# Performance work log

Measured on AMD Instinct MI355X. Metric: run time of the kernel, lower is better.

The kernel has to match this reference:

```python
import jax, jax.numpy as jnp
import numpy as np

D_MODEL = 1024
N_HEADS = 16
HEAD_DIM = D_MODEL // N_HEADS
D_FF = 4096
ROPE_RANK = 16
LN_EPS = 1e-5


def _ln(x, g, b):
    mu = jnp.mean(x, axis=-1, keepdims=True)
    var = jnp.mean((x - mu) ** 2, axis=-1, keepdims=True)
    return (x - mu) * jax.lax.rsqrt(var + LN_EPS) * g + b


def _rope(x, A, B_):
    # x: [B, T, D]; learned low-rank additive correction to sin/cos tables
    B, T, D = x.shape
    pos = jnp.arange(T, dtype=jnp.float32)
    theta = 1.0 / (10000.0 ** (jnp.arange(0, D, 2, dtype=jnp.float32) / D))  # [D/2]
    angles = pos[:, None] * theta[None, :]                                   # [T, D/2]
    sin_pos, cos_pos = jnp.sin(angles), jnp.cos(angles)
    base = jnp.concatenate([sin_pos, cos_pos], axis=-1)                      # [T, D]
    learned = (base @ A) @ B_                                                # [T, D]
    l_sin, l_cos = jnp.split(learned, 2, axis=-1)
    sin_f = sin_pos + l_sin                                                  # [T, D/2]
    cos_f = cos_pos + l_cos
    xe, xo = x[..., ::2], x[..., 1::2]
    re = xe * cos_f[None] - xo * sin_f[None]
    ro = xe * sin_f[None] + xo * cos_f[None]
    return jnp.stack([re, ro], axis=-1).reshape(B, T, D)


def setup_inputs() -> dict:
    key = jax.random.key(0)
    ks = jax.random.split(key, 20)
    B, T = 2, 2048
    s = 1.0 / np.sqrt(D_MODEL)
    sf = 1.0 / np.sqrt(D_FF)
    sr = 1.0 / np.sqrt(ROPE_RANK)
    return {
        "tgt": jax.random.normal(ks[0], (B, T, D_MODEL), jnp.float32),
        "Wq": jax.random.normal(ks[1], (D_MODEL, D_MODEL), jnp.float32) * s,
        "bq": jnp.zeros((D_MODEL,), jnp.float32),
        "Wk": jax.random.normal(ks[2], (D_MODEL, D_MODEL), jnp.float32) * s,
        "bk": jnp.zeros((D_MODEL,), jnp.float32),
        "Wv": jax.random.normal(ks[3], (D_MODEL, D_MODEL), jnp.float32) * s,
        "bv": jnp.zeros((D_MODEL,), jnp.float32),
        "Wo": jax.random.normal(ks[4], (D_MODEL, D_MODEL), jnp.float32) * s,
        "bo": jnp.zeros((D_MODEL,), jnp.float32),
        "W1": jax.random.normal(ks[5], (D_MODEL, D_FF), jnp.float32) * s,
        "b1": jnp.zeros((D_FF,), jnp.float32),
        "W2": jax.random.normal(ks[6], (D_FF, D_MODEL), jnp.float32) * sf,
        "b2": jnp.zeros((D_MODEL,), jnp.float32),
        "ln1_g": jnp.ones((D_MODEL,), jnp.float32),
        "ln1_b": jnp.zeros((D_MODEL,), jnp.float32),
        "ln2_g": jnp.ones((D_MODEL,), jnp.float32),
        "ln2_b": jnp.zeros((D_MODEL,), jnp.float32),
        "rope_A": jax.random.normal(ks[7], (D_MODEL, ROPE_RANK), jnp.float32) * s,
        "rope_B": jax.random.normal(ks[8], (ROPE_RANK, D_MODEL), jnp.float32) * sr,
    }


def reference(tgt, Wq, bq, Wk, bk, Wv, bv, Wo, bo, W1, b1, W2, b2,
              ln1_g, ln1_b, ln2_g, ln2_b, rope_A, rope_B):
    x = tgt
    B, T, D = x.shape
    q = _rope(x @ Wq + bq, rope_A, rope_B)
    k = _rope(x @ Wk + bk, rope_A, rope_B)
    v = x @ Wv + bv
    # [B, H, T, hd]
    q = q.reshape(B, T, N_HEADS, HEAD_DIM).transpose(0, 2, 1, 3)
    k = k.reshape(B, T, N_HEADS, HEAD_DIM).transpose(0, 2, 1, 3)
    v = v.reshape(B, T, N_HEADS, HEAD_DIM).transpose(0, 2, 1, 3)
    scores = jnp.einsum("bhqd,bhkd->bhqk", q, k) / np.sqrt(HEAD_DIM)
    attn = jax.nn.softmax(scores, axis=-1)  # no mask: module applies none
    ctx = jnp.einsum("bhqk,bhkd->bhqd", attn, v)
    ctx = ctx.transpose(0, 2, 1, 3).reshape(B, T, D)
    x = x + (ctx @ Wo + bo)
    x = _ln(x, ln1_g, ln1_b)
    ff = jax.nn.relu(x @ W1 + b1) @ W2 + b2
    x = _ln(x + ff, ln2_g, ln2_b)
    return x
```

## Files before the change

### kernel.cpp

```cpp
#include <hip/hip_runtime.h>
#include <math.h>

typedef unsigned short u16;
typedef unsigned int u32;
typedef __attribute__((ext_vector_type(8))) short short8v;
typedef __attribute__((ext_vector_type(4))) float f32x4;

__device__ __forceinline__ u16 f2bf(float f) {
    u32 u = __float_as_uint(f);
    u32 r = (u + 0x7fffu + ((u >> 16) & 1u)) >> 16;
    return (u16)r;
}

#define GLOAD_LDS(g, l)                                                        \
    __builtin_amdgcn_global_load_lds(                                          \
        (const __attribute__((address_space(1))) void*)(g),                    \
        (__attribute__((address_space(3))) void*)(l), 16, 0, 0)

#define SCHED_FENCE() __builtin_amdgcn_sched_barrier(0)

__global__ void cast_k(const float* __restrict__ x, u16* __restrict__ y) {
    const int gid = blockIdx.x * blockDim.x + threadIdx.x;
    float4 v = ((const float4*)x)[gid];
    ushort4 o;
    o.x = f2bf(v.x); o.y = f2bf(v.y); o.z = f2bf(v.z); o.w = f2bf(v.w);
    ((ushort4*)y)[gid] = o;
}

__global__ __launch_bounds__(256) void tcast_k(const float* __restrict__ S,
                                               u16* __restrict__ Dt,
                                               int K, int N) {
    __shared__ float tile[32][33];
    const int n0 = blockIdx.x * 32, k0 = blockIdx.y * 32;
    const int tx = threadIdx.x & 31, ty = threadIdx.x >> 5;
#pragma unroll
    for (int i = 0; i < 4; i++)
        tile[ty + 8 * i][tx] = S[(size_t)(k0 + ty + 8 * i) * N + n0 + tx];
    __syncthreads();
#pragma unroll
    for (int i = 0; i < 4; i++)
        Dt[(size_t)(n0 + ty + 8 * i) * K + k0 + tx] = f2bf(tile[tx][ty + 8 * i]);
}

__global__ __launch_bounds__(256) void vtrans_k(const u16* __restrict__ vv,
                                                u16* __restrict__ Vt) {
    __shared__ u16 tile[32][33];
    const int key0 = blockIdx.x * 32, d0 = blockIdx.y * 32, bh = blockIdx.z;
    const int b = bh >> 4, h = bh & 15;
    const int tx = threadIdx.x & 31, ty = threadIdx.x >> 5;
#pragma unroll
    for (int i = 0; i < 4; i++)
        tile[ty + 8 * i][tx] =
            vv[(size_t)(b * 2048 + key0 + ty + 8 * i) * 1024 + h * 64 + d0 + tx];
    __syncthreads();
#pragma unroll
    for (int i = 0; i < 4; i++) {
        const int d = d0 + ty + 8 * i;
        const int key = key0 + tx;
        const int ksw = (key & ~63) | ((((key >> 3) & 7) ^ (d & 7)) << 3) | (key & 7);
        Vt[((size_t)bh * 64 + d) * 2048 + ksw] = tile[tx][ty + 8 * i];
    }
}

#define ROPE_LOG2C (13.287712379549449f / 512.0f)

__global__ __launch_bounds__(256) void rope1_k(const float* __restrict__ A,
                                               float* __restrict__ P) {
    __shared__ float sc[16][17];
    __shared__ float cc[16][17];
    __shared__ float Als[16][17];
    __shared__ float Alc[16][17];
    const int tid = threadIdx.x;
    const int tt = tid >> 4, rr = tid & 15;
    const int t = blockIdx.x * 16 + tt;
    float acc = 0.f;
    for (int i0 = 0; i0 < 512; i0 += 16) {
        __syncthreads();
        {
            const int i = i0 + rr;
            const float th = exp2f(-(float)i * ROPE_LOG2C);
            const float ang = (float)t * th;
            sc[tt][rr] = sinf(ang);
            cc[tt][rr] = cosf(ang);
            Als[tt][rr] = A[(i0 + tt) * 16 + rr];
            Alc[tt][rr] = A[(512 + i0 + tt) * 16 + rr];
        }
        __syncthreads();
#pragma unroll
        for (int ii = 0; ii < 16; ++ii)
            acc = fmaf(sc[tt][ii], Als[ii][rr],
                       fmaf(cc[tt][ii], Alc[ii][rr], acc));
    }
    P[t * 16 + rr] = acc;
}

__global__ void rope2_k(const float* __restrict__ P, const float* __restrict__ Bw,
                        float* __restrict__ sf, float* __restrict__ cf) {
    const int gid = blockIdx.x * blockDim.x + threadIdx.x;
    if (gid >= 2048 * 512) return;
    const int t = gid >> 9, i = gid & 511;
    float ls = 0.f, lc = 0.f;
#pragma unroll
    for (int r = 0; r < 16; ++r) {
        const float p = P[t * 16 + r];
        ls = fmaf(p, Bw[r * 1024 + i], ls);
        lc = fmaf(p, Bw[r * 1024 + 512 + i], lc);
    }
    const float th = exp2f(-(float)i * ROPE_LOG2C);
    const float ang = (float)t * th;
    sf[gid] = sinf(ang) + ls;
    cf[gid] = cosf(ang) + lc;
}

__device__ __forceinline__ void xcd_tile(int L, int xn, int rn, int rm,
                                         int& tm, int& tn) {
    const int xcd = L & 7, i = L >> 3;
    const int cx = xcd % xn, cy = xcd / xn;
    tn = cx * rn + (i % rn);
    tm = cy * rm + (i / rn);
}

enum { EP_NONE = 0, EP_RES = 2, EP_RELU = 3 };

template <int EPI, bool CBF, int BN>
__global__ __launch_bounds__(256) void mgemm_k(
    const u16* __restrict__ A, const u16* __restrict__ Bt,
    const float* __restrict__ bias, const float* __restrict__ resf,
    void* __restrict__ Cp, int M, int N, int K, int xn, int rn, int rm) {
    constexpr int NT = BN / 32;
    __shared__ u16 As[3 * 128 * 32];
    __shared__ u16 Bs[3 * BN * 32];
    const int tid = threadIdx.x;
    const int w = tid >> 6, l = tid & 63;
    const int quad = l >> 4, lr = l & 15;
    const int wr = w >> 1, wc = w & 1;
    int tm, tn;
    xcd_tile(blockIdx.x, xn, rn, rm, tm, tn);
    const int m0 = tm * 128, n0 = tn * BN;

    const int srow = w * 16 + (l >> 2);
    const int scol = (((l & 3) ^ ((l >> 3) & 3)) * 8);
    const u16* ag0 = A + (size_t)(m0 + srow) * K + scol;
    const u16* ag1 = A + (size_t)(m0 + 64 + srow) * K + scol;
    const u16* bg0 = Bt + (size_t)(n0 + srow) * K + scol;
    const u16* bg1 = Bt + (size_t)(n0 + 64 + srow) * K + scol;

    f32x4 acc[4][NT];
#pragma unroll
    for (int i = 0; i < 4; i++)
#pragma unroll
        for (int j = 0; j < NT; j++) acc[i][j] = (f32x4)(0.0f);

    {
        GLOAD_LDS(ag0, As + w * 512);
        GLOAD_LDS(ag1, As + 2048 + w * 512);
        GLOAD_LDS(bg0, Bs + w * 512);
        if (BN == 128) GLOAD_LDS(bg1, Bs + 2048 + w * 512);
        GLOAD_LDS(ag0 + 32, As + 4096 + w * 512);
        GLOAD_LDS(ag1 + 32, As + 4096 + 2048 + w * 512);
        GLOAD_LDS(bg0 + 32, Bs + BN * 32 + w * 512);
        if (BN == 128) GLOAD_LDS(bg1 + 32, Bs + BN * 32 + 2048 + w * 512);
    }

    const int niter = K >> 5;
    const int xsw = ((lr >> 1) & 3) << 3;
    int bc = 0, bs = 2;
    for (int i = 0; i < niter; ++i) {
        SCHED_FENCE();
        if (i + 1 < niter) {
            if (BN == 128) asm volatile("s_waitcnt vmcnt(4) lgkmcnt(0)" ::: "memory");
            else           asm volatile("s_waitcnt vmcnt(3) lgkmcnt(0)" ::: "memory");
        } else {
            asm volatile("s_waitcnt vmcnt(0) lgkmcnt(0)" ::: "memory");
        }
        __builtin_amdgcn_s_barrier();
        SCHED_FENCE();
        if (i + 2 < niter) {
            const int kk = (i + 2) << 5;
            u16* Ab = As + bs * 4096;
            u16* Bb = Bs + bs * (BN * 32);
            GLOAD_LDS(ag0 + kk, Ab + w * 512);
            GLOAD_LDS(ag1 + kk, Ab + 2048 + w * 512);
            GLOAD_LDS(bg0 + kk, Bb + w * 512);
            if (BN == 128) GLOAD_LDS(bg1 + kk, Bb + 2048 + w * 512);
        }
        const u16* Ac = As + bc * 4096;
        const u16* Bc = Bs + bc * (BN * 32);
        short8v af[4], bf[NT];
#pragma unroll
        for (int mt = 0; mt < 4; ++mt)
            af[mt] = *(const short8v*)&Ac[(wr * 64 + mt * 16 + lr) * 32 +
                                          ((quad << 3) ^ xsw)];
#pragma unroll
        for (int nt = 0; nt < NT; ++nt)
            bf[nt] = *(const short8v*)&Bc[(wc * (BN / 2) + nt * 16 + lr) * 32 +
                                          ((quad << 3) ^ xsw)];
#pragma unroll
        for (int mt = 0; mt < 4; ++mt)
#pragma unroll
            for (int nt = 0; nt < NT; ++nt)
                acc[mt][nt] = __builtin_amdgcn_mfma_f32_16x16x32_bf16(
                    af[mt], bf[nt], acc[mt][nt], 0, 0, 0);
        bc = (bc == 2) ? 0 : bc + 1;
        bs = (bs == 2) ? 0 : bs + 1;
    }

#pragma unroll
    for (int mt = 0; mt < 4; ++mt) {
#pragma unroll
        for (int nt = 0; nt < NT; ++nt) {
            const int n = n0 + wc * (BN / 2) + nt * 16 + lr;
            const float bb = bias[n];
#pragma unroll
            for (int reg = 0; reg < 4; ++reg) {
                const int m = m0 + wr * 64 + mt * 16 + quad * 4 + reg;
                float v = acc[mt][nt][reg] + bb;
                if (EPI == EP_RES) v += resf[(size_t)m * N + n];
                if (EPI == EP_RELU) v = fmaxf(v, 0.f);
                if (CBF) ((u16*)Cp)[(size_t)m * N + n] = f2bf(v);
                else     ((float*)Cp)[(size_t)m * N + n] = v;
            }
        }
    }
}

__global__ __launch_bounds__(256) void mqkv_k(
    const u16* __restrict__ A, const u16* __restrict__ Bt,
    const float* __restrict__ bq, const float* __restrict__ bk,
    const float* __restrict__ bv, const float* __restrict__ sf,
    const float* __restrict__ cf, u16* __restrict__ out) {
    const int K = 1024;
    __shared__ u16 As[3 * 128 * 32];
    __shared__ u16 Bs[3 * 128 * 32];
    const int tid = threadIdx.x;
    const int w = tid >> 6, l = tid & 63;
    const int quad = l >> 4, lr = l & 15;
    const int wr = w >> 1, wc = w & 1;
    int tm, tn;
    xcd_tile(blockIdx.x, 4, 6, 16, tm, tn);
    const int m0 = tm * 128, n0 = tn * 128;

    const int srow = w * 16 + (l >> 2);
    const int scol = (((l & 3) ^ ((l >> 3) & 3)) * 8);
    const u16* ag0 = A + (size_t)(m0 + srow) * K + scol;
    const u16* ag1 = A + (size_t)(m0 + 64 + srow) * K + scol;
    const u16* bg0 = Bt + (size_t)(n0 + srow) * K + scol;
    const u16* bg1 = Bt + (size_t)(n0 + 64 + srow) * K + scol;

    f32x4 acc[4][4];
#pragma unroll
    for (int i = 0; i < 4; i++)
#pragma unroll
        for (int j = 0; j < 4; j++) acc[i][j] = (f32x4)(0.0f);

    {
        GLOAD_LDS(ag0, As + w * 512);
        GLOAD_LDS(ag1, As + 2048 + w * 512);
        GLOAD_LDS(bg0, Bs + w * 512);
        GLOAD_LDS(bg1, Bs + 2048 + w * 512);
        GLOAD_LDS(ag0 + 32, As + 4096 + w * 512);
        GLOAD_LDS(ag1 + 32, As + 4096 + 2048 + w * 512);
        GLOAD_LDS(bg0 + 32, Bs + 4096 + w * 512);
        GLOAD_LDS(bg1 + 32, Bs + 4096 + 2048 + w * 512);
    }
    const int xsw = ((lr >> 1) & 3) << 3;
    int bc = 0, bsb = 2;
    for (int i = 0; i < 32; ++i) {
        SCHED_FENCE();
        if (i + 1 < 32) {
            asm volatile("s_waitcnt vmcnt(4) lgkmcnt(0)" ::: "memory");
        } else {
            asm volatile("s_waitcnt vmcnt(0) lgkmcnt(0)" ::: "memory");
        }
        __builtin_amdgcn_s_barrier();
        SCHED_FENCE();
        if (i + 2 < 32) {
            const int kk = (i + 2) << 5;
            u16* Ab = As + bsb * 4096;
            u16* Bb = Bs + bsb * 4096;
            GLOAD_LDS(ag0 + kk, Ab + w * 512);
            GLOAD_LDS(ag1 + kk, Ab + 2048 + w * 512);
            GLOAD_LDS(bg0 + kk, Bb + w * 512);
            GLOAD_LDS(bg1 + kk, Bb + 2048 + w * 512);
        }
        const u16* Ac = As + bc * 4096;
        const u16* Bc = Bs + bc * 4096;
        short8v af[4], bf[4];
#pragma unroll
        for (int mt = 0; mt < 4; ++mt)
            af[mt] = *(const short8v*)&Ac[(wr * 64 + mt * 16 + lr) * 32 +
                                          ((quad << 3) ^ xsw)];
#pragma unroll
        for (int nt = 0; nt < 4; ++nt)
            bf[nt] = *(const short8v*)&Bc[(wc * 64 + nt * 16 + lr) * 32 +
                                          ((quad << 3) ^ xsw)];
#pragma unroll
        for (int mt = 0; mt < 4; ++mt)
#pragma unroll
            for (int nt = 0; nt < 4; ++nt)
                acc[mt][nt] = __builtin_amdgcn_mfma_f32_16x16x32_bf16(
                    af[mt], bf[nt], acc[mt][nt], 0, 0, 0);
        bc = (bc == 2) ? 0 : bc + 1;
        bsb = (bsb == 2) ? 0 : bsb + 1;
    }

    const int which = n0 >> 10;
    const float* bias = which == 0 ? bq : (which == 1 ? bk : bv);
    const bool doRope = which < 2;
    u16* Cp = out + (size_t)which * 4096 * 1024;

#pragma unroll
    for (int mt = 0; mt < 4; ++mt) {
#pragma unroll
        for (int nt = 0; nt < 4; ++nt) {
            const int n = n0 + wc * 64 + nt * 16 + lr;
            const int col = n & 1023;
            const float bb = bias[col];
#pragma unroll
            for (int reg = 0; reg < 4; ++reg) {
                const int m = m0 + wr * 64 + mt * 16 + quad * 4 + reg;
                float v = acc[mt][nt][reg] + bb;
                const float partner = __shfl_xor(v, 1);
                int colw = col;
                if (doRope) {
                    const int t = m & 2047;
                    const int fi = col >> 1;
                    const float svv = sf[t * 512 + fi];
                    const float cvv = cf[t * 512 + fi];
                    v = (col & 1) ? fmaf(partner, svv, v * cvv)
                                  : fmaf(v, cvv, -partner * svv);
                    if (which == 0) v *= 0.125f;
                    colw = (col & ~63) | ((((col >> 3) & 7) ^ (m & 7)) << 3) |
                           (col & 7);
                }
                Cp[(size_t)m * 1024 + colw] = f2bf(v);
            }
        }
    }
}

__global__ __launch_bounds__(256, 3) void mattn_k(
    const u16* __restrict__ Q, const u16* __restrict__ Kg,
    const u16* __restrict__ Vt, u16* __restrict__ O) {
    __shared__ u16 QPs[128 * 64];
    __shared__ u16 Ks[2][64 * 64];
    __shared__ u16 Vs[2][64 * 64];
    const int tid = threadIdx.x;
    const int w = tid >> 6, l = tid & 63;
    const int quad = l >> 4, lr = l & 15;
    const int L = blockIdx.x;
    const int bh = (L & 7) * 4 + ((L >> 3) & 3);
    const int b = bh >> 4, h = bh & 15;
    const int row0 = (L >> 5) * 128;
    const size_t base = (size_t)b * 2048 * 1024 + (size_t)h * 64;
    const size_t vbase = (size_t)bh * 64 * 2048;

    const int dr = l >> 3;
    const int dc = (l & 7) * 8;
    const int g0 = w * 2, g1 = g0 + 1;
    const u16* kg0 = Kg + base + (size_t)(g0 * 8 + dr) * 1024 + dc;
    const u16* kg1 = Kg + base + (size_t)(g1 * 8 + dr) * 1024 + dc;
    const u16* vg0 = Vt + vbase + (size_t)(g0 * 8 + dr) * 2048 + dc;
    const u16* vg1 = Vt + vbase + (size_t)(g1 * 8 + dr) * 2048 + dc;

#pragma unroll
    for (int j = 0; j < 4; ++j) {
        const int g = w * 4 + j;
        GLOAD_LDS(Q + base + (size_t)(row0 + g * 8 + dr) * 1024 + dc,
                  QPs + g * 512);
    }
    GLOAD_LDS(kg0, Ks[0] + g0 * 512);
    GLOAD_LDS(kg1, Ks[0] + g1 * 512);
    GLOAD_LDS(vg0, Vs[0] + g0 * 512);
    GLOAD_LDS(vg1, Vs[0] + g1 * 512);
    __syncthreads();

    const int rsw = lr & 7;
    short8v qf[2][2];
#pragma unroll
    for (int ntq = 0; ntq < 2; ++ntq) {
        const int qr = w * 32 + ntq * 16 + lr;
#pragma unroll
        for (int kh = 0; kh < 2; ++kh)
            qf[ntq][kh] = *(const short8v*)&QPs[qr * 64 +
                (((kh * 4 + quad) ^ rsw) << 3)];
    }

    f32x4 o_acc[2][4];
#pragma unroll
    for (int i = 0; i < 2; ++i)
#pragma unroll
        for (int j = 0; j < 4; ++j) o_acc[i][j] = (f32x4)(0.0f);
    float lsum[2] = {0.f, 0.f};

    for (int i = 0; i < 32; ++i) {
        __syncthreads();
        if (i + 1 < 32) {
            const size_t kro = (size_t)((i + 1) << 6) * 1024;
            const int kco = (i + 1) << 6;
            u16* Kb = Ks[(i + 1) & 1];
            u16* Vb = Vs[(i + 1) & 1];
            GLOAD_LDS(kg0 + kro, Kb + g0 * 512);
            GLOAD_LDS(kg1 + kro, Kb + g1 * 512);
            GLOAD_LDS(vg0 + kco, Vb + g0 * 512);
            GLOAD_LDS(vg1 + kco, Vb + g1 * 512);
        }
        const u16* Kc = Ks[i & 1];
        const u16* Vc = Vs[i & 1];

        f32x4 s[4][2];
#pragma unroll
        for (int mt = 0; mt < 4; ++mt)
#pragma unroll
            for (int ntq = 0; ntq < 2; ++ntq) s[mt][ntq] = (f32x4)(0.0f);
#pragma unroll
        for (int mt = 0; mt < 4; ++mt) {
            const int kr = mt * 16 + lr;
            const short8v kf0 = *(const short8v*)&Kc[kr * 64 + ((quad ^ rsw) << 3)];
            const short8v kf1 = *(const short8v*)&Kc[kr * 64 + (((quad + 4) ^ rsw) << 3)];
#pragma unroll
            for (int ntq = 0; ntq < 2; ++ntq) {
                s[mt][ntq] = __builtin_amdgcn_mfma_f32_16x16x32_bf16(
                    kf0, qf[ntq][0], s[mt][ntq], 0, 0, 0);
                s[mt][ntq] = __builtin_amdgcn_mfma_f32_16x16x32_bf16(
                    kf1, qf[ntq][1], s[mt][ntq], 0, 0, 0);
            }
        }

#pragma unroll
        for (int ntq = 0; ntq < 2; ++ntq) {
            const int prow = w * 32 + ntq * 16 + lr;
#pragma unroll
            for (int mt = 0; mt < 4; ++mt) {
                const float e0 = __expf(s[mt][ntq][0]);
                const float e1 = __expf(s[mt][ntq][1]);
                const float e2 = __expf(s[mt][ntq][2]);
                const float e3 = __expf(s[mt][ntq][3]);
                lsum[ntq] += (e0 + e1) + (e2 + e3);
                u32 p01, p23;
                asm("v_cvt_pk_bf16_f32 %0, %1, %2" : "=v"(p01) : "v"(e0), "v"(e1));
                asm("v_cvt_pk_bf16_f32 %0, %1, %2" : "=v"(p23) : "v"(e2), "v"(e3));
                uint2 pv; pv.x = p01; pv.y = p23;
                *(uint2*)&QPs[prow * 64 +
                              (((mt * 2 + (quad >> 1)) ^ rsw) << 3) +
                              (quad & 1) * 4] = pv;
            }
        }

        short8v vf[4][2];
#pragma unroll
        for (int ntd = 0; ntd < 4; ++ntd) {
            const int vr = ntd * 16 + lr;
            vf[ntd][0] = *(const short8v*)&Vc[vr * 64 + ((quad ^ rsw) << 3)];
            vf[ntd][1] = *(const short8v*)&Vc[vr * 64 + (((quad + 4) ^ rsw) << 3)];
        }
        short8v pf[2][2];
#pragma unroll
        for (int mtq = 0; mtq < 2; ++mtq) {
            const int prow = w * 32 + mtq * 16 + lr;
            pf[mtq][0] = *(const short8v*)&QPs[prow * 64 + ((quad ^ rsw) << 3)];
            pf[mtq][1] = *(const short8v*)&QPs[prow * 64 + (((quad + 4) ^ rsw) << 3)];
        }
#pragma unroll
        for (int mtq = 0; mtq < 2; ++mtq)
#pragma unroll
            for (int ntd = 0; ntd < 4; ++ntd) {
                o_acc[mtq][ntd] = __builtin_amdgcn_mfma_f32_16x16x32_bf16(
                    pf[mtq][0], vf[ntd][0], o_acc[mtq][ntd], 0, 0, 0);
                o_acc[mtq][ntd] = __builtin_amdgcn_mfma_f32_16x16x32_bf16(
                    pf[mtq][1], vf[ntd][1], o_acc[mtq][ntd], 0, 0, 0);
            }
    }

    float rden[2];
#pragma unroll
    for (int ntq = 0; ntq < 2; ++ntq) {
        float t = lsum[ntq];
        t += __shfl_xor(t, 16);
        t += __shfl_xor(t, 32);
        rden[ntq] = 1.0f / t;
    }
#pragma unroll
    for (int mtq = 0; mtq < 2; ++mtq) {
#pragma unroll
        for (int reg = 0; reg < 4; ++reg) {
            const float dsc = __shfl(rden[mtq], quad * 4 + reg);
            const int m = row0 + w * 32 + mtq * 16 + quad * 4 + reg;
#pragma unroll
            for (int ntd = 0; ntd < 4; ++ntd)
                O[base + (size_t)m * 1024 + ntd * 16 + lr] =
                    f2bf(o_acc[mtq][ntd][reg] * dsc);
        }
    }
}

__global__ __launch_bounds__(256) void ln_k(
    const float* __restrict__ X, const float* __restrict__ g,
    const float* __restrict__ bb, float* __restrict__ outf,
    u16* __restrict__ outb) {
    const int row = blockIdx.x, tid = threadIdx.x;
    const float* x = X + (size_t)row * 1024;
    float4 xv = *(const float4*)&x[tid * 4];
    float s = xv.x + xv.y + xv.z + xv.w;
    float s2 = xv.x * xv.x + xv.y * xv.y + xv.z * xv.z + xv.w * xv.w;
#pragma unroll
    for (int msk = 32; msk >= 1; msk >>= 1) {
        s += __shfl_xor(s, msk);
        s2 += __shfl_xor(s2, msk);
    }
    __shared__ float red[8];
    const int wv = tid >> 6;
    if ((tid & 63) == 0) { red[wv] = s; red[wv + 4] = s2; }
    __syncthreads();
    s = red[0] + red[1] + red[2] + red[3];
    s2 = red[4] + red[5] + red[6] + red[7];
    const float mu = s * (1.f / 1024.f);
    float var = s2 * (1.f / 1024.f) - mu * mu;
    var = fmaxf(var, 0.f);
    const float rstd = rsqrtf(var + 1e-5f);
    float4 g4 = *(const float4*)&g[tid * 4];
    float4 b4 = *(const float4*)&bb[tid * 4];
    float o0 = (xv.x - mu) * rstd * g4.x + b4.x;
    float o1 = (xv.y - mu) * rstd * g4.y + b4.y;
    float o2 = (xv.z - mu) * rstd * g4.z + b4.z;
    float o3 = (xv.w - mu) * rstd * g4.w + b4.w;
    if (outf)
        *(float4*)(outf + (size_t)row * 1024 + tid * 4) = make_float4(o0, o1, o2, o3);
    if (outb) {
        ushort4 ov;
        ov.x = f2bf(o0); ov.y = f2bf(o1); ov.z = f2bf(o2); ov.w = f2bf(o3);
        *(ushort4*)(outb + (size_t)row * 1024 + tid * 4) = ov;
    }
}

extern "C" void kernel_launch(void* const* d_in, const int* in_sizes, int n_in,
                              void* d_out, int out_size, void* d_ws, size_t ws_size,
                              hipStream_t stream) {
    const float* tgt = (const float*)d_in[0];
    const float* Wq  = (const float*)d_in[1];
    const float* bq  = (const float*)d_in[2];
    const float* Wk  = (const float*)d_in[3];
    const float* bk  = (const float*)d_in[4];
    const float* Wv  = (const float*)d_in[5];
    const float* bv  = (const float*)d_in[6];
    const float* Wo  = (const float*)d_in[7];
    const float* bo  = (const float*)d_in[8];
    const float* W1  = (const float*)d_in[9];
    const float* b1  = (const float*)d_in[10];
    const float* W2  = (const float*)d_in[11];
    const float* b2  = (const float*)d_in[12];
    const float* g1  = (const float*)d_in[13];
    const float* be1 = (const float*)d_in[14];
    const float* g2  = (const float*)d_in[15];
    const float* be2 = (const float*)d_in[16];
    const float* rA  = (const float*)d_in[17];
    const float* rB  = (const float*)d_in[18];

    const int M = 4096, D = 1024, DFF = 4096;
    const size_t MD = (size_t)M * D;
    const size_t MB = 1u << 20;
    char* wsb = (char*)d_ws;

    u16* q    = (u16*)wsb;
    u16* vv   = q + 2 * MD;
    u16* ctx  = q + 3 * MD;
    u16* h    = q;
    float* x1  = (float*)(wsb + 32 * MB);
    float* sfp = (float*)(wsb + 48 * MB);
    float* cfp = sfp + (size_t)2048 * 512;
    u16* x1b  = (u16*)sfp;
    u16* tgtb = (u16*)(wsb + 56 * MB);
    u16* Vt   = (u16*)(wsb + 56 * MB);
    u16* Wqt  = (u16*)(wsb + 64 * MB);
    u16* Wkt  = (u16*)(wsb + 66 * MB);
    u16* Wvt  = (u16*)(wsb + 68 * MB);
    u16* Wot  = (u16*)(wsb + 70 * MB);
    u16* W1t  = (u16*)(wsb + 72 * MB);
    u16* W2t  = (u16*)(wsb + 80 * MB);
    float* Pp = (float*)(wsb + 88 * MB);

    cast_k<<<dim3(4096), dim3(256), 0, stream>>>(tgt, tgtb);
    tcast_k<<<dim3(32, 32),  dim3(256), 0, stream>>>(Wq, Wqt, D, D);
    tcast_k<<<dim3(32, 32),  dim3(256), 0, stream>>>(Wk, Wkt, D, D);
    tcast_k<<<dim3(32, 32),  dim3(256), 0, stream>>>(Wv, Wvt, D, D);
    tcast_k<<<dim3(32, 32),  dim3(256), 0, stream>>>(Wo, Wot, D, D);
    tcast_k<<<dim3(128, 32), dim3(256), 0, stream>>>(W1, W1t, D, DFF);
    tcast_k<<<dim3(32, 128), dim3(256), 0, stream>>>(W2, W2t, DFF, D);
    rope1_k<<<dim3(128), dim3(256), 0, stream>>>(rA, Pp);
    rope2_k<<<dim3(4096), dim3(256), 0, stream>>>(Pp, rB, sfp, cfp);

    mqkv_k<<<dim3(768), dim3(256), 0, stream>>>(
        tgtb, Wqt, bq, bk, bv, sfp, cfp, q);

    vtrans_k<<<dim3(64, 2, 32), dim3(256), 0, stream>>>(vv, Vt);

    mattn_k<<<dim3(512), dim3(256), 0, stream>>>(q, q + MD, Vt, ctx);

    mgemm_k<EP_RES, false, 64><<<dim3(512), dim3(256), 0, stream>>>(
        ctx, Wot, bo, tgt, x1, M, D, D, 2, 8, 8);
    ln_k<<<dim3(4096), dim3(256), 0, stream>>>(x1, g1, be1, x1, x1b);
    mgemm_k<EP_RELU, true, 128><<<dim3(1024), dim3(256), 0, stream>>>(
        x1b, W1t, b1, nullptr, h, M, DFF, D, 4, 8, 16);
    mgemm_k<EP_RES, false, 64><<<dim3(512), dim3(256), 0, stream>>>(
        h, W2t, b2, x1, x1, M, D, DFF, 2, 8, 8);
    ln_k<<<dim3(4096), dim3(256), 0, stream>>>(x1, g2, be2, (float*)d_out, nullptr);

    (void)in_sizes; (void)n_in; (void)out_size; (void)ws_size;
}
```

Before: 446.5 us.

## Split-K the Wo and W2 GEMMs and fuse partial reduction into LayerNorm

The output-projection and FFN-down GEMMs now use 128-wide N tiles with K split in two halves. This keeps the same block count while each tile reuses operands more. The two fp32 partial results go to separate buffers. Bias, residual add and the sum of the two partials are folded into the LayerNorm kernel, and the workspace layout is reshuffled so the partial buffers reuse dead regions. In exchange the GEMMs write extra fp32 partial traffic that the LayerNorm pass must read back.

```diff
diff --git a/kernel.cpp b/kernel.cpp
--- a/kernel.cpp
+++ b/kernel.cpp
@@ -120,13 +120,14 @@
     tm = cy * rm + (i / rn);
 }
 
-enum { EP_NONE = 0, EP_RES = 2, EP_RELU = 3 };
+enum { EP_NONE = 0, EP_RELU = 3, EP_PART = 4 };
 
 template <int EPI, bool CBF, int BN>
 __global__ __launch_bounds__(256) void mgemm_k(
     const u16* __restrict__ A, const u16* __restrict__ Bt,
-    const float* __restrict__ bias, const float* __restrict__ resf,
-    void* __restrict__ Cp, int M, int N, int K, int xn, int rn, int rm) {
+    const float* __restrict__ bias, void* __restrict__ Cp,
+    void* __restrict__ Cp2, int M, int N, int K, int lda, int ldb,
+    int xn, int rn, int rm, int mtiles) {
     constexpr int NT = BN / 32;
     __shared__ u16 As[3 * 128 * 32];
     __shared__ u16 Bs[3 * BN * 32];
@@ -136,14 +137,19 @@
     const int wr = w >> 1, wc = w & 1;
     int tm, tn;
     xcd_tile(blockIdx.x, xn, rn, rm, tm, tn);
+    int kh = 0;
+    if (tm >= mtiles) { kh = 1; tm -= mtiles; }
+    const u16* Ak = A + (size_t)kh * K;
+    const u16* Bk = Bt + (size_t)kh * K;
+    void* Co = kh ? Cp2 : Cp;
     const int m0 = tm * 128, n0 = tn * BN;
 
     const int srow = w * 16 + (l >> 2);
     const int scol = (((l & 3) ^ ((l >> 3) & 3)) * 8);
-    const u16* ag0 = A + (size_t)(m0 + srow) * K + scol;
-    const u16* ag1 = A + (size_t)(m0 + 64 + srow) * K + scol;
-    const u16* bg0 = Bt + (size_t)(n0 + srow) * K + scol;
-    const u16* bg1 = Bt + (size_t)(n0 + 64 + srow) * K + scol;
+    const u16* ag0 = Ak + (size_t)(m0 + srow) * lda + scol;
+    const u16* ag1 = Ak + (size_t)(m0 + 64 + srow) * lda + scol;
+    const u16* bg0 = Bk + (size_t)(n0 + srow) * ldb + scol;
+    const u16* bg1 = Bk + (size_t)(n0 + 64 + srow) * ldb + scol;
 
     f32x4 acc[4][NT];
 #pragma unroll
@@ -210,15 +216,14 @@
 #pragma unroll
         for (int nt = 0; nt < NT; ++nt) {
             const int n = n0 + wc * (BN / 2) + nt * 16 + lr;
-            const float bb = bias[n];
+            const float bb = (EPI == EP_PART) ? 0.0f : bias[n];
 #pragma unroll
             for (int reg = 0; reg < 4; ++reg) {
                 const int m = m0 + wr * 64 + mt * 16 + quad * 4 + reg;
                 float v = acc[mt][nt][reg] + bb;
-                if (EPI == EP_RES) v += resf[(size_t)m * N + n];
                 if (EPI == EP_RELU) v = fmaxf(v, 0.f);
-                if (CBF) ((u16*)Cp)[(size_t)m * N + n] = f2bf(v);
-                else     ((float*)Cp)[(size_t)m * N + n] = v;
+                if (CBF) ((u16*)Co)[(size_t)m * N + n] = f2bf(v);
+                else     ((float*)Co)[(size_t)m * N + n] = v;
             }
         }
     }
@@ -494,13 +499,21 @@
     }
 }
 
-__global__ __launch_bounds__(256) void ln_k(
-    const float* __restrict__ X, const float* __restrict__ g,
-    const float* __restrict__ bb, float* __restrict__ outf,
-    u16* __restrict__ outb) {
+__global__ __launch_bounds__(256) void lnf_k(
+    const float* __restrict__ X, const float* __restrict__ P0,
+    const float* __restrict__ P1, const float* __restrict__ cb,
+    const float* __restrict__ g, const float* __restrict__ bb,
+    float* __restrict__ outf, u16* __restrict__ outb) {
     const int row = blockIdx.x, tid = threadIdx.x;
-    const float* x = X + (size_t)row * 1024;
-    float4 xv = *(const float4*)&x[tid * 4];
+    const size_t off = (size_t)row * 1024 + tid * 4;
+    float4 xv = *(const float4*)&X[off];
+    float4 p0 = *(const float4*)&P0[off];
+    float4 p1 = *(const float4*)&P1[off];
+    float4 c4 = *(const float4*)&cb[tid * 4];
+    xv.x += p0.x + p1.x + c4.x;
+    xv.y += p0.y + p1.y + c4.y;
+    xv.z += p0.z + p1.z + c4.z;
+    xv.w += p0.w + p1.w + c4.w;
     float s = xv.x + xv.y + xv.z + xv.w;
     float s2 = xv.x * xv.x + xv.y * xv.y + xv.z * xv.z + xv.w * xv.w;
 #pragma unroll
@@ -525,11 +538,11 @@
     float o2 = (xv.z - mu) * rstd * g4.z + b4.z;
     float o3 = (xv.w - mu) * rstd * g4.w + b4.w;
     if (outf)
-        *(float4*)(outf + (size_t)row * 1024 + tid * 4) = make_float4(o0, o1, o2, o3);
+        *(float4*)(outf + off) = make_float4(o0, o1, o2, o3);
     if (outb) {
         ushort4 ov;
         ov.x = f2bf(o0); ov.y = f2bf(o1); ov.z = f2bf(o2); ov.w = f2bf(o3);
-        *(ushort4*)(outb + (size_t)row * 1024 + tid * 4) = ov;
+        *(ushort4*)(outb + off) = ov;
     }
 }
 
@@ -563,21 +576,25 @@
 
     u16* q    = (u16*)wsb;
     u16* vv   = q + 2 * MD;
-    u16* ctx  = q + 3 * MD;
+    u16* ctx  = (u16*)(wsb + 16 * MB);
+    u16* Vt   = (u16*)(wsb + 24 * MB);
     u16* h    = q;
-    float* x1  = (float*)(wsb + 32 * MB);
-    float* sfp = (float*)(wsb + 48 * MB);
+    float* PW0 = (float*)wsb;
+    float* PW1 = (float*)(wsb + 32 * MB);
+    float* PF0 = (float*)(wsb + 64 * MB);
+    float* PF1 = (float*)(wsb + 32 * MB);
+    float* sfp = (float*)(wsb + 32 * MB);
     float* cfp = sfp + (size_t)2048 * 512;
-    u16* x1b  = (u16*)sfp;
-    u16* tgtb = (u16*)(wsb + 56 * MB);
-    u16* Vt   = (u16*)(wsb + 56 * MB);
+    u16* tgtb = (u16*)(wsb + 40 * MB);
+    float* x1  = (float*)(wsb + 48 * MB);
+    u16* x1b  = (u16*)(wsb + 64 * MB);
     u16* Wqt  = (u16*)(wsb + 64 * MB);
     u16* Wkt  = (u16*)(wsb + 66 * MB);
     u16* Wvt  = (u16*)(wsb + 68 * MB);
     u16* Wot  = (u16*)(wsb + 70 * MB);
     u16* W1t  = (u16*)(wsb + 72 * MB);
     u16* W2t  = (u16*)(wsb + 80 * MB);
-    float* Pp = (float*)(wsb + 88 * MB);
+    float* Pp = (float*)wsb;
 
     cast_k<<<dim3(4096), dim3(256), 0, stream>>>(tgt, tgtb);
     tcast_k<<<dim3(32, 32),  dim3(256), 0, stream>>>(Wq, Wqt, D, D);
@@ -596,14 +613,16 @@
 
     mattn_k<<<dim3(512), dim3(256), 0, stream>>>(q, q + MD, Vt, ctx);
 
-    mgemm_k<EP_RES, false, 64><<<dim3(512), dim3(256), 0, stream>>>(
-        ctx, Wot, bo, tgt, x1, M, D, D, 2, 8, 8);
-    ln_k<<<dim3(4096), dim3(256), 0, stream>>>(x1, g1, be1, x1, x1b);
+    mgemm_k<EP_PART, false, 128><<<dim3(512), dim3(256), 0, stream>>>(
+        ctx, Wot, nullptr, PW0, PW1, M, D, 512, D, D, 1, 8, 8, 32);
+    lnf_k<<<dim3(4096), dim3(256), 0, stream>>>(
+        tgt, PW0, PW1, bo, g1, be1, x1, x1b);
     mgemm_k<EP_RELU, true, 128><<<dim3(1024), dim3(256), 0, stream>>>(
-        x1b, W1t, b1, nullptr, h, M, DFF, D, 4, 8, 16);
-    mgemm_k<EP_RES, false, 64><<<dim3(512), dim3(256), 0, stream>>>(
-        h, W2t, b2, x1, x1, M, D, DFF, 2, 8, 8);
-    ln_k<<<dim3(4096), dim3(256), 0, stream>>>(x1, g2, be2, (float*)d_out, nullptr);
+        x1b, W1t, b1, h, nullptr, M, DFF, D, D, D, 4, 8, 16, 1 << 20);
+    mgemm_k<EP_PART, false, 128><<<dim3(512), dim3(256), 0, stream>>>(
+        h, W2t, nullptr, PF0, PF1, M, D, 2048, DFF, DFF, 1, 8, 8, 32);
+    lnf_k<<<dim3(4096), dim3(256), 0, stream>>>(
+        x1, PF0, PF1, b2, g2, be2, (float*)d_out, nullptr);
 
     (void)in_sizes; (void)n_in; (void)out_size; (void)ws_size;
 }
```

Result: faster. 428.4 us (-4.0%).
